# Kernel tuning notes

Measured on AMD Instinct MI355X. Metric: run time of the kernel, lower is better.

## Reference

```python
import jax, jax.numpy as jnp
import numpy as np

B, N, E, H = 4, 2048, 768, 8
D = E // H
SCALING = D ** (-0.5)


def setup_inputs() -> dict:
    key = jax.random.key(0)
    k0, k1, k2, k3, k4 = jax.random.split(key, 5)
    x = jax.random.normal(k0, (B, N, E), dtype=jnp.float32)
    Wqkv = jax.random.normal(k1, (E, 3 * E), dtype=jnp.float32) * 0.02
    bqkv = jax.random.normal(k2, (3 * E,), dtype=jnp.float32) * 0.02
    Wproj = jax.random.normal(k3, (E, E), dtype=jnp.float32) * 0.02
    bproj = jax.random.normal(k4, (E,), dtype=jnp.float32) * 0.02
    return {"x": x, "Wqkv": Wqkv, "bqkv": bqkv, "Wproj": Wproj, "bproj": bproj}


def reference(x, Wqkv, bqkv, Wproj, bproj):
    b, n, e = x.shape
    h, d = H, E // H
    # QKV projection: [b, n, 3e]
    qkv = x @ Wqkv + bqkv
    # rearrange 'b n (h d qkv) -> qkv b h n d': qkv is the INNERMOST axis
    qkv = qkv.reshape(b, n, h, d, 3)
    q = jnp.transpose(qkv[..., 0], (0, 2, 1, 3))  # [b, h, n, d]
    k = jnp.transpose(qkv[..., 1], (0, 2, 1, 3))
    v = jnp.transpose(qkv[..., 2], (0, 2, 1, 3))
    # unscaled attention scores, softmax, then post-softmax scaling (as in source)
    energy = jnp.einsum('bhqd,bhkd->bhqk', q, k)  # [b, h, n, n]
    att = jax.nn.softmax(energy, axis=-1) * SCALING
    out = jnp.einsum('bhqk,bhkd->bhqd', att, v)   # [b, h, n, d]
    out = jnp.transpose(out, (0, 2, 1, 3)).reshape(b, n, e)
    return out @ Wproj + bproj
```

## Files before the change

### kernel.cpp

```cpp
#include <hip/hip_runtime.h>
#include <cstdint>

#define BB 4
#define SEQ 2048
#define EMB 768
#define NH 8
#define HD 96
#define E3 2304
#define MTOK 8192
#define NROWS 65536
#define KSPLIT 4
#define SCALING 0.10206207261596575f
#define LOG2E 1.44269504f

typedef unsigned short u16;
typedef unsigned int u32;
typedef __bf16 bf16x8 __attribute__((ext_vector_type(8)));
typedef float f32x4 __attribute__((ext_vector_type(4)));
typedef float f32x16 __attribute__((ext_vector_type(16)));

__device__ __forceinline__ u16 f2bf(float f) {
    union { float f; uint32_t u; } c; c.f = f;
    uint32_t u = c.u;
    return (u16)((u + 0x7FFFu + ((u >> 16) & 1u)) >> 16);
}
__device__ __forceinline__ uint32_t pk2(float a, float b) {
    return (uint32_t)f2bf(a) | ((uint32_t)f2bf(b) << 16);
}
__device__ __forceinline__ uint32_t cvtpk(float a, float b) {
    uint32_t r;
    asm("v_cvt_pk_bf16_f32 %0, %1, %2" : "=v"(r) : "v"(a), "v"(b));
    return r;
}
__device__ __forceinline__ float bf2f(u16 h) {
    union { uint32_t u; float f; } c; c.u = ((uint32_t)h) << 16; return c.f;
}
__device__ __forceinline__ float fexp2(float x) {
    return __builtin_amdgcn_exp2f(x);
}
__device__ __forceinline__ void async16(const u16* g, u16* l) {
    __builtin_amdgcn_global_load_lds(
        (const __attribute__((address_space(1))) void*)g,
        (__attribute__((address_space(3))) void*)l, 16, 0, 0);
}


__device__ __forceinline__ void transpose_body(const float* __restrict__ src,
                                               u16* __restrict__ dst,
                                               int ncols, int mode, int j0, int k0,
                                               int tid, float (*T)[65]) {
#pragma unroll
    for (int it = 0; it < 16; ++it) {
        int lin = it * 256 + tid;
        int rr2 = lin >> 6, jj = lin & 63;
        int j = j0 + jj;
        int c;
        if (mode == 0) c = j;
        else if (mode == 1) { int s = j / 768, rr = j % 768; c = (rr / 96) * 288 + (rr % 96) * 3 + s; }
        else { c = (j / 96) * 288 + (j % 96) * 3 + 2; }
        T[rr2][jj] = src[(k0 + rr2) * ncols + c];
    }
    __syncthreads();
#pragma unroll
    for (int it = 0; it < 16; ++it) {
        int lin = it * 256 + tid;
        int jr = lin >> 6, kc = lin & 63;
        dst[(size_t)(j0 + jr) * 768 + k0 + kc] = f2bf(T[kc][jr]);
    }
}

__global__ __launch_bounds__(256) void prep_kernel(const float* __restrict__ x,
                                                   const float* __restrict__ Wqkv,
                                                   const float* __restrict__ Wproj,
                                                   u16* __restrict__ xb,
                                                   u16* __restrict__ wqkT,
                                                   u16* __restrict__ wvr,
                                                   u16* __restrict__ wpt) {
    __shared__ float T[64][65];
    int bid = blockIdx.x, tid = threadIdx.x;
    if (bid < 3072) {
        int i = bid * 256 + tid;
        const float4* s4 = (const float4*)x;
        float4 a = s4[2 * i];
        float4 c = s4[2 * i + 1];
        uint4 o;
        o.x = pk2(a.x, a.y); o.y = pk2(a.z, a.w);
        o.z = pk2(c.x, c.y); o.w = pk2(c.z, c.w);
        ((uint4*)xb)[i] = o;
    } else if (bid < 3360) {
        int t = bid - 3072;
        transpose_body(Wqkv, wqkT, E3, 1, (t % 24) * 64, (t / 24) * 64, tid, T);
    } else if (bid < 3504) {
        int t = bid - 3360;
        transpose_body(Wqkv, wvr, E3, 2, (t % 12) * 64, (t / 12) * 64, tid, T);
    } else {
        int t = bid - 3504;
        transpose_body(Wproj, wpt, EMB, 0, (t % 12) * 64, (t / 12) * 64, tid, T);
    }
}


__device__ __forceinline__ void gemm_tiles(const u16* __restrict__ A,
                                           const u16* __restrict__ Bt,
                                           int m0, int n0, int tid,
                                           u16* As, u16* Bs, f32x4 acc[4][4]) {
    const int lane = tid & 63;
    const int w = tid >> 6;
    const int l15 = lane & 15;
    const int quad = lane >> 4;
    const int wr = (w >> 1) * 64;
    const int wc = (w & 1) * 64;
    const int swz = l15 & 7;
    for (int kb = 0; kb < 768; kb += 64) {
#pragma unroll
        for (int it = 0; it < 4; ++it) {
            int base = (w * 4 + it) * 64;
            int lin = base + lane;
            int row = lin >> 3, cl = lin & 7;
            int cg = cl ^ (row & 7);
            async16(&A[(size_t)(m0 + row) * 768 + kb + cg * 8], &As[base * 8]);
            async16(&Bt[(size_t)(n0 + row) * 768 + kb + cg * 8], &Bs[base * 8]);
        }
        __syncthreads();
#pragma unroll
        for (int ks = 0; ks < 2; ++ks) {
            bf16x8 af[4], bfg[4];
#pragma unroll
            for (int fi = 0; fi < 4; ++fi)
                af[fi] = *(const bf16x8*)&As[(wr + fi * 16 + l15) * 64 + (((ks * 4 + quad) ^ swz) * 8)];
#pragma unroll
            for (int fj = 0; fj < 4; ++fj)
                bfg[fj] = *(const bf16x8*)&Bs[(wc + fj * 16 + l15) * 64 + (((ks * 4 + quad) ^ swz) * 8)];
#pragma unroll
            for (int fi = 0; fi < 4; ++fi)
#pragma unroll
                for (int fj = 0; fj < 4; ++fj)
                    acc[fi][fj] = __builtin_amdgcn_mfma_f32_16x16x32_bf16(af[fi], bfg[fj], acc[fi][fj], 0, 0, 0);
        }
        __syncthreads();
    }
}

__device__ __forceinline__ void gemm_tiles64(const u16* __restrict__ A,
                                             const u16* __restrict__ Bt,
                                             int m0, int n0, int tid,
                                             u16* As, u16* Bs, f32x4 acc[4][2]) {
    const int lane = tid & 63;
    const int w = tid >> 6;
    const int l15 = lane & 15;
    const int quad = lane >> 4;
    const int wr = (w >> 1) * 64;
    const int wc = (w & 1) * 32;
    const int swz = l15 & 7;
    for (int kb = 0; kb < 768; kb += 64) {
#pragma unroll
        for (int it = 0; it < 4; ++it) {
            int base = (w * 4 + it) * 64;
            int lin = base + lane;
            int row = lin >> 3, cl = lin & 7;
            int cg = cl ^ (row & 7);
            async16(&A[(size_t)(m0 + row) * 768 + kb + cg * 8], &As[base * 8]);
        }
#pragma unroll
        for (int it = 0; it < 2; ++it) {
            int base = (w * 2 + it) * 64;
            int lin = base + lane;
            int row = lin >> 3, cl = lin & 7;
            int cg = cl ^ (row & 7);
            async16(&Bt[(size_t)(n0 + row) * 768 + kb + cg * 8], &Bs[base * 8]);
        }
        __syncthreads();
#pragma unroll
        for (int ks = 0; ks < 2; ++ks) {
            bf16x8 af[4], bfg[2];
#pragma unroll
            for (int fi = 0; fi < 4; ++fi)
                af[fi] = *(const bf16x8*)&As[(wr + fi * 16 + l15) * 64 + (((ks * 4 + quad) ^ swz) * 8)];
#pragma unroll
            for (int fj = 0; fj < 2; ++fj)
                bfg[fj] = *(const bf16x8*)&Bs[(wc + fj * 16 + l15) * 64 + (((ks * 4 + quad) ^ swz) * 8)];
#pragma unroll
            for (int fi = 0; fi < 4; ++fi)
#pragma unroll
                for (int fj = 0; fj < 2; ++fj)
                    acc[fi][fj] = __builtin_amdgcn_mfma_f32_16x16x32_bf16(af[fi], bfg[fj], acc[fi][fj], 0, 0, 0);
        }
        __syncthreads();
    }
}

__global__ __launch_bounds__(256) void gemm_qkv_kernel(const u16* __restrict__ xb,
                                                       const u16* __restrict__ wqkT,
                                                       const u16* __restrict__ wvr,
                                                       const float* __restrict__ bqkv,
                                                       u16* __restrict__ qb,
                                                       u16* __restrict__ kg,
                                                       u16* __restrict__ vt) {
    __shared__ __align__(16) u16 As[128 * 64];
    __shared__ __align__(16) u16 Bs[128 * 64];
    int bid = blockIdx.x, tid = threadIdx.x;
    int lane = tid & 63, w = tid >> 6, l15 = lane & 15, quad = lane >> 4;
    if (bid < 768) {
        int n0 = (bid % 12) * 128, m0 = (bid / 12) * 128;
        f32x4 acc[4][4] = {};
        gemm_tiles(xb, wqkT, m0, n0, tid, As, Bs, acc);
        int wr = (w >> 1) * 64, wc = (w & 1) * 64;
#pragma unroll
        for (int fj = 0; fj < 4; ++fj) {
            int j = n0 + wc + fj * 16 + l15;
            int s = j / 768, rr = j % 768;
            int hh = rr / 96, dd = rr % 96;
            float bv = bqkv[hh * 288 + dd * 3 + s];
#pragma unroll
            for (int fi = 0; fi < 4; ++fi) {
#pragma unroll
                for (int r = 0; r < 4; ++r) {
                    int m = m0 + wr + fi * 16 + quad * 4 + r;
                    int b = m >> 11, n = m & 2047;
                    int bh = b * NH + hh;
                    float v = acc[fi][fj][r] + bv;
                    if (s == 0) {
                        qb[((size_t)bh * SEQ + n) * HD + dd] = f2bf(v * LOG2E);
                    } else {
                        int cp = (dd >> 3) ^ (n & 7);
                        kg[((size_t)bh * SEQ + n) * 128 + cp * 8 + (dd & 7)] = f2bf(v);
                    }
                }
            }
        }
    } else {
        int t = bid - 768;
        int n0 = (t % 128) * 64, m0 = (t / 128) * 128;
        f32x4 acc[4][2] = {};
        gemm_tiles64(wvr, xb, m0, n0, tid, As, Bs, acc);
        int wr = (w >> 1) * 64, wc = (w & 1) * 32;
        float bvs[4][4]; int hhs[4][4], dds[4][4];
#pragma unroll
        for (int fi = 0; fi < 4; ++fi)
#pragma unroll
            for (int r = 0; r < 4; ++r) {
                int m = m0 + wr + fi * 16 + quad * 4 + r;
                int hh = m / 96, dd = m % 96;
                hhs[fi][r] = hh; dds[fi][r] = dd;
                bvs[fi][r] = bqkv[hh * 288 + dd * 3 + 2];
            }
#pragma unroll
        for (int fj = 0; fj < 2; ++fj) {
            int n = n0 + wc + fj * 16 + l15;
            int b = n >> 11, nn = n & 2047;
#pragma unroll
            for (int fi = 0; fi < 4; ++fi) {
#pragma unroll
                for (int r = 0; r < 4; ++r) {
                    int dd = dds[fi][r];
                    int kk = (nn & ~63) | ((((nn >> 3) ^ dd) & 7) << 3) | (nn & 7);
                    vt[((size_t)(b * NH + hhs[fi][r]) * HD + dd) * SEQ + kk] =
                        f2bf(acc[fi][fj][r] + bvs[fi][r]);
                }
            }
        }
    }
}

__global__ __launch_bounds__(256) void gemm_proj_kernel(const u16* __restrict__ A,
                                                        const u16* __restrict__ Bt,
                                                        const float* __restrict__ bias,
                                                        float* __restrict__ out) {
    __shared__ __align__(16) u16 As[128 * 64];
    __shared__ __align__(16) u16 Bs[64 * 64];
    int tid = threadIdx.x;
    int n0 = blockIdx.x * 64, m0 = blockIdx.y * 128;
    f32x4 acc[4][2] = {};
    gemm_tiles64(A, Bt, m0, n0, tid, As, Bs, acc);
    int lane = tid & 63, w = tid >> 6, l15 = lane & 15, quad = lane >> 4;
    int wr = (w >> 1) * 64, wc = (w & 1) * 32;
#pragma unroll
    for (int fj = 0; fj < 2; ++fj) {
        int j = n0 + wc + fj * 16 + l15;
        float bv = bias[j];
#pragma unroll
        for (int fi = 0; fi < 4; ++fi) {
#pragma unroll
            for (int r = 0; r < 4; ++r) {
                int m = m0 + wr + fi * 16 + quad * 4 + r;
                out[(size_t)m * 768 + j] = acc[fi][fj][r] + bv;
            }
        }
    }
}

__global__ __launch_bounds__(512, 4) void attn_kernel(const u16* __restrict__ Q,
                                                      const u16* __restrict__ Kg,
                                                      const u16* __restrict__ Vt,
                                                      u16* __restrict__ part,
                                                      float* __restrict__ lpart) {
    __shared__ __align__(16) u16 Ks[64 * 128];
    __shared__ __align__(16) u16 Vs[96 * 64];
    int tid = threadIdx.x;
    int lane = tid & 63, w = tid >> 6;
    int l31 = lane & 31, hf = lane >> 5;
    int swz = l31 & 7;
    int bid = blockIdx.x;
    int qt = bid >> 7;
    int g = bid & 127;
    int bh = g >> 2, kh = g & 3;
    const u16* qp = Q + (size_t)bh * SEQ * HD;
    const u16* kgp = Kg + (size_t)bh * SEQ * 128;
    const u16* vtp = Vt + (size_t)bh * HD * SEQ;
    int qbase = qt * 256 + w * 32;
    int kbase = kh * 512;

    bf16x8 aq[6];
#pragma unroll
    for (int dc = 0; dc < 6; ++dc)
        aq[dc] = *(const bf16x8*)&qp[(size_t)(qbase + l31) * HD + dc * 16 + hf * 8];

    f32x16 Ot[3] = {};
    float lp = 0.f;

    for (int kt = 0; kt < 8; ++kt) {
        int k0 = kbase + kt * 64;
#pragma unroll
        for (int it = 0; it < 2; ++it) {
            int cw = w * 2 + it;
            async16(kgp + (size_t)(k0 + cw * 4 + (lane >> 4)) * 128 + (lane & 15) * 8,
                    &Ks[cw * 512]);
        }
#pragma unroll
        for (int it = 0; it < 2; ++it) {
            int vw = it * 8 + w;
            if (vw < 12)
                async16(vtp + (size_t)(vw * 8 + (lane >> 3)) * SEQ + k0 + (lane & 7) * 8,
                        &Vs[vw * 512]);
        }
        __syncthreads();

#pragma unroll
        for (int tau = 0; tau < 2; ++tau) {
            f32x16 Sv = {};
            __builtin_amdgcn_s_setprio(1);
#pragma unroll
            for (int dc = 0; dc < 6; ++dc) {
                bf16x8 ka = *(const bf16x8*)&Ks[(tau * 32 + l31) * 128 + (((2 * dc + hf) ^ swz) * 8)];
                Sv = __builtin_amdgcn_mfma_f32_32x32x16_bf16(ka, aq[dc], Sv, 0, 0, 0);
            }
            __builtin_amdgcn_s_setprio(0);
            u32 pk[4][2];
#pragma unroll
            for (int g2 = 0; g2 < 4; ++g2)
#pragma unroll
                for (int u = 0; u < 2; ++u) {
                    float a0 = fexp2(Sv[g2 * 4 + 2 * u]);
                    float a1 = fexp2(Sv[g2 * 4 + 2 * u + 1]);
                    lp += a0 + a1;
                    pk[g2][u] = cvtpk(a0, a1);
                }
#pragma unroll
            for (int kc = 0; kc < 2; ++kc)
#pragma unroll
                for (int u = 0; u < 2; ++u)
                    asm("v_permlane32_swap_b32 %0, %1"
                        : "+v"(pk[2 * kc][u]), "+v"(pk[2 * kc + 1][u]));
#pragma unroll
            for (int kc = 0; kc < 2; ++kc) {
                union { u32 u[4]; bf16x8 v; } pf;
                pf.u[0] = pk[2 * kc][0];     pf.u[1] = pk[2 * kc][1];
                pf.u[2] = pk[2 * kc + 1][0]; pf.u[3] = pk[2 * kc + 1][1];
                __builtin_amdgcn_s_setprio(1);
#pragma unroll
                for (int t = 0; t < 3; ++t) {
                    bf16x8 va = *(const bf16x8*)&Vs[(t * 32 + l31) * 64 + (((4 * tau + 2 * kc + hf) ^ swz) * 8)];
                    Ot[t] = __builtin_amdgcn_mfma_f32_32x32x16_bf16(va, pf.v, Ot[t], 0, 0, 0);
                }
                __builtin_amdgcn_s_setprio(0);
            }
        }
        __syncthreads();
    }

    size_t pb = (size_t)kh * NROWS + (size_t)bh * SEQ;
    {
        int q = qbase + l31;
        float lr = lp + __shfl_xor(lp, 32);
        if (hf == 0) lpart[pb + q] = lr;
        size_t rowb = (pb + q) * HD;
#pragma unroll
        for (int t = 0; t < 3; ++t) {
#pragma unroll
            for (int g2 = 0; g2 < 4; ++g2) {
                int d0 = t * 32 + 8 * g2 + 4 * hf;
                uint2 val;
                val.x = pk2(Ot[t][g2 * 4 + 0], Ot[t][g2 * 4 + 1]);
                val.y = pk2(Ot[t][g2 * 4 + 2], Ot[t][g2 * 4 + 3]);
                *(uint2*)&part[rowb + d0] = val;
            }
        }
    }
}

__global__ __launch_bounds__(256) void combine_kernel(const u16* __restrict__ part,
                                                      const float* __restrict__ lpart,
                                                      u16* __restrict__ ao) {
    int idx = blockIdx.x * 256 + threadIdx.x;
    int row = idx / 12, ch = idx % 12;
    float l = 0.f;
#pragma unroll
    for (int k = 0; k < KSPLIT; ++k) l += lpart[(size_t)k * NROWS + row];
    float sc = SCALING / l;
    float acc[8] = {};
#pragma unroll
    for (int k = 0; k < KSPLIT; ++k) {
        uint4 pv = *(const uint4*)&part[((size_t)k * NROWS + row) * HD + ch * 8];
        const u16* a = (const u16*)&pv;
#pragma unroll
        for (int i = 0; i < 8; ++i) acc[i] += bf2f(a[i]);
    }
    uint4 o;
    u32* ou = (u32*)&o;
#pragma unroll
    for (int i = 0; i < 4; ++i)
        ou[i] = pk2(acc[2 * i] * sc, acc[2 * i + 1] * sc);
    int bh = row >> 11, n = row & 2047;
    int b = bh >> 3, h = bh & 7;
    *(uint4*)&ao[((size_t)(b * SEQ + n)) * EMB + h * HD + ch * 8] = o;
}


extern "C" void kernel_launch(void* const* d_in, const int* in_sizes, int n_in,
                              void* d_out, int out_size, void* d_ws, size_t ws_size,
                              hipStream_t stream) {
    const float* x     = (const float*)d_in[0];
    const float* Wqkv  = (const float*)d_in[1];
    const float* bqkv  = (const float*)d_in[2];
    const float* Wproj = (const float*)d_in[3];
    const float* bproj = (const float*)d_in[4];
    float* out = (float*)d_out;

    char* p = (char*)d_ws;
    u16*   qb    = (u16*)p;  p += (size_t)NROWS * HD * 2;
    u16*   kg    = (u16*)p;  p += (size_t)NROWS * 128 * 2;
    u16*   vt    = (u16*)p;  p += (size_t)NROWS * HD * 2;
    u16*   ao    = (u16*)p;  p += (size_t)MTOK * EMB * 2;
    u16*   wpt   = (u16*)p;  p += (size_t)EMB * EMB * 2;
    float* lpart = (float*)p; p += (size_t)KSPLIT * NROWS * 4;
    char*  U     = p;
    u16*   xb    = (u16*)U;
    u16*   wqkT  = (u16*)(U + (size_t)MTOK * EMB * 2);
    u16*   wvr   = (u16*)(U + (size_t)MTOK * EMB * 2 + (size_t)1536 * EMB * 2);
    u16*   partb = (u16*)U;

    prep_kernel<<<3648, 256, 0, stream>>>(x, Wqkv, Wproj, xb, wqkT, wvr, wpt);
    gemm_qkv_kernel<<<1536, 256, 0, stream>>>(xb, wqkT, wvr, bqkv, qb, kg, vt);
    attn_kernel<<<8 * 32 * KSPLIT, 512, 0, stream>>>(qb, kg, vt, partb, lpart);
    combine_kernel<<<NROWS * 12 / 256, 256, 0, stream>>>(partb, lpart, ao);
    gemm_proj_kernel<<<dim3(EMB / 64, MTOK / 128), 256, 0, stream>>>(ao, wpt, bproj, out);
}
```

Before: 238.2 us.

## Unify QKV GEMM into single 128x128 tiling and scatter V transposed

Replaces the two-branch QKV kernel, which ran a separate transposed 128x64 GEMM for V, with one uniform 128x128 tile grid over all 2304 output columns. The V columns are read from the weight rows that sit directly after the Q/K weights in workspace, and are written with a transposed, swizzled scatter. This cuts block count and removes the less efficient 64-wide tiles. In exchange, V stores are now strided across rows of the transposed buffer, so they are less coalesced.

```diff
diff --git a/kernel.cpp b/kernel.cpp
--- a/kernel.cpp
+++ b/kernel.cpp
@@ -191,20 +191,19 @@
 
 __global__ __launch_bounds__(256) void gemm_qkv_kernel(const u16* __restrict__ xb,
                                                        const u16* __restrict__ wqkT,
-                                                       const u16* __restrict__ wvr,
                                                        const float* __restrict__ bqkv,
                                                        u16* __restrict__ qb,
                                                        u16* __restrict__ kg,
                                                        u16* __restrict__ vt) {
     __shared__ __align__(16) u16 As[128 * 64];
     __shared__ __align__(16) u16 Bs[128 * 64];
-    int bid = blockIdx.x, tid = threadIdx.x;
+    int tid = threadIdx.x;
+    int n0 = blockIdx.x * 128, m0 = blockIdx.y * 128;
+    f32x4 acc[4][4] = {};
+    gemm_tiles(xb, wqkT, m0, n0, tid, As, Bs, acc);
     int lane = tid & 63, w = tid >> 6, l15 = lane & 15, quad = lane >> 4;
-    if (bid < 768) {
-        int n0 = (bid % 12) * 128, m0 = (bid / 12) * 128;
-        f32x4 acc[4][4] = {};
-        gemm_tiles(xb, wqkT, m0, n0, tid, As, Bs, acc);
-        int wr = (w >> 1) * 64, wc = (w & 1) * 64;
+    int wr = (w >> 1) * 64, wc = (w & 1) * 64;
+    if (n0 < 1536) {
 #pragma unroll
         for (int fj = 0; fj < 4; ++fj) {
             int j = n0 + wc + fj * 16 + l15;
@@ -229,33 +228,21 @@
             }
         }
     } else {
-        int t = bid - 768;
-        int n0 = (t % 128) * 64, m0 = (t / 128) * 128;
-        f32x4 acc[4][2] = {};
-        gemm_tiles64(wvr, xb, m0, n0, tid, As, Bs, acc);
-        int wr = (w >> 1) * 64, wc = (w & 1) * 32;
-        float bvs[4][4]; int hhs[4][4], dds[4][4];
-#pragma unroll
-        for (int fi = 0; fi < 4; ++fi)
-#pragma unroll
-            for (int r = 0; r < 4; ++r) {
-                int m = m0 + wr + fi * 16 + quad * 4 + r;
-                int hh = m / 96, dd = m % 96;
-                hhs[fi][r] = hh; dds[fi][r] = dd;
-                bvs[fi][r] = bqkv[hh * 288 + dd * 3 + 2];
-            }
-#pragma unroll
-        for (int fj = 0; fj < 2; ++fj) {
-            int n = n0 + wc + fj * 16 + l15;
-            int b = n >> 11, nn = n & 2047;
+#pragma unroll
+        for (int fj = 0; fj < 4; ++fj) {
+            int c = n0 + wc + fj * 16 + l15 - 1536;
+            int hh = c / 96, dd = c % 96;
+            float bv = bqkv[hh * 288 + dd * 3 + 2];
+            size_t rowb = ((size_t)hh * HD + dd) * SEQ;
 #pragma unroll
             for (int fi = 0; fi < 4; ++fi) {
 #pragma unroll
                 for (int r = 0; r < 4; ++r) {
-                    int dd = dds[fi][r];
+                    int m = m0 + wr + fi * 16 + quad * 4 + r;
+                    int b = m >> 11, nn = m & 2047;
                     int kk = (nn & ~63) | ((((nn >> 3) ^ dd) & 7) << 3) | (nn & 7);
-                    vt[((size_t)(b * NH + hhs[fi][r]) * HD + dd) * SEQ + kk] =
-                        f2bf(acc[fi][fj][r] + bvs[fi][r]);
+                    vt[(size_t)b * NH * HD * SEQ + rowb + kk] =
+                        f2bf(acc[fi][fj][r] + bv);
                 }
             }
         }
@@ -450,7 +437,7 @@
     u16*   partb = (u16*)U;
 
     prep_kernel<<<3648, 256, 0, stream>>>(x, Wqkv, Wproj, xb, wqkT, wvr, wpt);
-    gemm_qkv_kernel<<<1536, 256, 0, stream>>>(xb, wqkT, wvr, bqkv, qb, kg, vt);
+    gemm_qkv_kernel<<<dim3(E3 / 128, MTOK / 128), 256, 0, stream>>>(xb, wqkT, bqkv, qb, kg, vt);
     attn_kernel<<<8 * 32 * KSPLIT, 512, 0, stream>>>(qb, kg, vt, partb, lpart);
     combine_kernel<<<NROWS * 12 / 256, 256, 0, stream>>>(partb, lpart, ao);
     gemm_proj_kernel<<<dim3(EMB / 64, MTOK / 128), 256, 0, stream>>>(ao, wpt, bproj, out);
```

Measured after the change: 237.0 us. About the same (-0.5%).
